# Kernel tuning notes

Hardware: AMD Instinct MI355X
Metric: run time of the kernel (lower is better)

The kernel has to match this reference:

```python
import jax, jax.numpy as jnp
import numpy as np

M = 1024       # molecules
A = 24         # atoms per molecule
N = M * A      # total atoms
H = 128        # hidden_channels
F = 128        # num_filters
G = 50         # num_gaussians
T = 3          # num_interactions
CUTOFF = 10.0
LOG2 = float(np.log(2.0))


def setup_inputs() -> dict:
    key = jax.random.key(0)
    ks = jax.random.split(key, 20)
    z = jax.random.randint(ks[0], (N,), 1, 10)
    # each molecule's atoms in a 5A box -> max pair dist 8.66 < cutoff, all pairs connected
    pos = jax.random.uniform(ks[1], (N, 3), dtype=jnp.float32) * 5.0
    batch = jnp.repeat(jnp.arange(M), A)
    # dense intra-molecule radius graph (deterministic shape)
    i = np.arange(A)
    s, d = np.meshgrid(i, i, indexing='ij')
    m = s != d
    s, d = s[m], d[m]                      # [A*(A-1)]
    offs = (np.arange(M) * A)[:, None]
    edge_index = jnp.asarray(np.stack([(offs + s[None]).ravel(),
                                       (offs + d[None]).ravel()]).astype(np.int64))
    nrm = lambda k, shape: jax.random.normal(k, shape, dtype=jnp.float32) * 0.05
    params = dict(
        emb=nrm(ks[2], (100, H)),
        mlp_w1=nrm(ks[3], (T, G, F)), mlp_b1=jnp.zeros((T, F), jnp.float32),
        mlp_w2=nrm(ks[4], (T, F, F)), mlp_b2=jnp.zeros((T, F), jnp.float32),
        lin1_w=nrm(ks[5], (T, H, F)),
        lin2_w=nrm(ks[6], (T, F, H)), lin2_b=jnp.zeros((T, H), jnp.float32),
        lin_w=nrm(ks[7], (T, H, H)), lin_b=jnp.zeros((T, H), jnp.float32),
        out_w1=nrm(ks[8], (H, H // 2)), out_b1=jnp.zeros((H // 2,), jnp.float32),
        out_w2=nrm(ks[9], (H // 2, 1)), out_b2=jnp.zeros((1,), jnp.float32),
    )
    return dict(z=z, pos=pos, batch=batch, edge_index=edge_index, **params)


def _ssp(x):  # shifted softplus
    return jax.nn.softplus(x) - LOG2


def reference(z, pos, batch, edge_index, emb,
              mlp_w1, mlp_b1, mlp_w2, mlp_b2,
              lin1_w, lin2_w, lin2_b, lin_w, lin_b,
              out_w1, out_b1, out_w2, out_b2):
    src, dst = edge_index[0], edge_index[1]          # message j->i: gather src, scatter dst
    h = emb[z]                                       # [N,H]
    diff = pos[src] - pos[dst]                       # [E,3]
    ew = jnp.sqrt(jnp.sum(diff * diff, axis=-1))     # [E] edge distances
    # Gaussian smearing
    offset = jnp.linspace(0.0, CUTOFF, G, dtype=jnp.float32)
    coeff = -0.5 / (offset[1] - offset[0]) ** 2
    ea = jnp.exp(coeff * (ew[:, None] - offset) ** 2)   # [E,G]
    # cosine cutoff
    C = 0.5 * (jnp.cos(ew * (np.pi / CUTOFF)) + 1.0)    # [E]
    for t in range(T):
        W = _ssp(ea @ mlp_w1[t] + mlp_b1[t]) @ mlp_w2[t] + mlp_b2[t]  # [E,F]
        W = W * C[:, None]
        xf = h @ lin1_w[t]                            # [N,F]
        msg = xf[src] * W                             # [E,F]
        agg = jax.ops.segment_sum(msg, dst, num_segments=N)  # [N,F]
        v = _ssp(agg @ lin2_w[t] + lin2_b[t]) @ lin_w[t] + lin_b[t]  # [N,H]
        h = h + v                                     # residual
    h = _ssp(h @ out_w1 + out_b1)                     # [N,H/2]
    atom_e = h @ out_w2 + out_b2                      # [N,1]
    return jax.ops.segment_sum(atom_e, batch, num_segments=M)  # [M,1] readout='add'
```

## Files before the change

kernel.cpp:

```cpp
#include <hip/hip_runtime.h>
#include <math.h>

#define AT 24
#define ATP 32
#define HD 128
#define GD 50
#define NT 3
#define CUTOFF 10.0f
#define NK 1024

#define KP_W 136
#define XFP 132

#define SZ_BIG (128*KP_W)
#define WS_LIN1(t) ((t)*SZ_BIG)
#define WS_LIN2(t) ((3+(t))*SZ_BIG)
#define WS_LIN(t)  ((6+(t))*SZ_BIG)
#define WS_OW1     (9*SZ_BIG)
#define WS_TAB     (9*SZ_BIG + 64*KP_W)

typedef __attribute__((ext_vector_type(8))) short short8;
typedef __attribute__((ext_vector_type(4))) float f32x4;
typedef __attribute__((ext_vector_type(2))) float f32x2;

__device__ __forceinline__ unsigned short f2bf(float x) {
    unsigned int u = __float_as_uint(x);
    return (unsigned short)((u + 0x7fffu + ((u >> 16) & 1u)) >> 16);
}
__device__ __forceinline__ float sspf(float x) {
    return fmaxf(x, 0.0f) + __logf(1.0f + __expf(-fabsf(x))) - 0.69314718055994531f;
}

#if __has_builtin(__builtin_amdgcn_fdot2_f32_bf16)
typedef __attribute__((ext_vector_type(2))) __bf16 bfv2;
__device__ __forceinline__ float dot2bf(unsigned td, unsigned fp) {
    return __builtin_amdgcn_fdot2_f32_bf16(
        __builtin_bit_cast(bfv2, td), __builtin_bit_cast(bfv2, fp), 0.0f, false);
}
#else
__device__ __forceinline__ float dot2bf(unsigned td, unsigned fp) {
    float t = __uint_as_float(td << 16);
    float d = __uint_as_float(td & 0xFFFF0000u);
    float f = __uint_as_float(fp & 0xFFFF0000u);
    return fmaf(f, d, t);
}
#endif

__device__ __forceinline__ void g2l_async(const void* g, void* l, int bytes, int tid) {
    int w = tid >> 6, lane = tid & 63;
    const char* gc = (const char*)g + lane * 16;
    char* lc = (char*)l + lane * 16;
    for (int ofs = w * 1024; ofs < bytes; ofs += 8192) {
        __builtin_amdgcn_global_load_lds(
            (const __attribute__((address_space(1))) unsigned int*)(gc + ofs),
            (__attribute__((address_space(3))) unsigned int*)(lc + ofs), 16, 0, 0);
    }
}

__device__ __forceinline__ f32x4 mfma16(short8 a, short8 b, f32x4 c) {
    return __builtin_amdgcn_mfma_f32_16x16x32_bf16(a, b, c, 0, 0, 0);
}

template<int NKT>
__device__ __forceinline__ void gemm2(const unsigned short* A, const unsigned short* B,
                                      int q, f32x4* acc)
{
#pragma unroll
    for (int kt = 0; kt < NKT; ++kt) {
        short8 a  = *(const short8*)(A + kt * 32 + q * 8);
        short8 b0 = *(const short8*)(B + kt * 32 + q * 8);
        short8 b1 = *(const short8*)(B + 64 * KP_W + kt * 32 + q * 8);
        acc[0] = mfma16(a, b0, acc[0]);
        acc[1] = mfma16(a, b1, acc[1]);
    }
}

__global__ void __launch_bounds__(256) prep(
    const float* __restrict__ lin1_w, const float* __restrict__ lin2_w,
    const float* __restrict__ lin_w,  const float* __restrict__ out_w1,
    const float* __restrict__ mlp_w1, const float* __restrict__ mlp_b1,
    const float* __restrict__ mlp_w2, const float* __restrict__ mlp_b2,
    unsigned short* __restrict__ ws)
{
    int b = blockIdx.x, tid = threadIdx.x;
    if (b < 40) {
        const float* src; unsigned short* dst; int N, n0, rows;
        if (b < 36) {
            int mat = b >> 2, slice = b & 3;
            int grp = mat / 3, t = mat - grp * 3;
            const float* bases[3] = {lin1_w, lin2_w, lin_w};
            src = bases[grp] + t * HD * HD;
            dst = ws + (grp * 3 + t) * SZ_BIG;
            N = 128; n0 = slice * 32; rows = 32;
        } else {
            src = out_w1; dst = ws + WS_OW1; N = 64; n0 = (b - 36) * 16; rows = 16;
        }
        int nn = tid & 31, kk = tid >> 5;
        if (nn < rows) {
            for (int k = kk; k < KP_W; k += 8) {
                float v = (k < HD) ? src[k * N + n0 + nn] : 0.f;
                dst[(n0 + nn) * KP_W + k] = f2bf(v);
            }
        }
        return;
    }
    __shared__ __align__(16) float w2s[HD * HD];
    __shared__ __align__(16) float ea[9][52];
    __shared__ float pacc[4][5][128];
    __shared__ __align__(16) unsigned short tabst[8 * 256];

    int b2 = b - 40;
    int t = b2 >> 7, k0 = (b2 & 127) << 3;

    {
        const char* gc = (const char*)(mlp_w2 + t * HD * HD) + tid * 16;
        char* lc = (char*)w2s + tid * 16;
#pragma unroll
        for (int ofs = 0; ofs < 65536; ofs += 4096)
            __builtin_amdgcn_global_load_lds(
                (const __attribute__((address_space(1))) unsigned int*)(gc + ofs),
                (__attribute__((address_space(3))) unsigned int*)(lc + ofs), 16, 0, 0);
    }

    const float h = CUTOFF / (NK - 1);
    const float STEP = CUTOFF / (GD - 1);
    const float COEFF = -0.5f / (STEP * STEP);
    for (int i = tid; i < 9 * GD; i += 256) {
        int rr = i / GD, g = i - rr * GD;
        int k = min(k0 + rr, NK - 1);
        float r = (float)k * h;
        float d = r - (float)g * STEP;
        ea[rr][g] = __expf(COEFF * d * d);
    }
    __syncthreads();

    int j = tid & 127, kh = tid >> 7;
    float pre[5];
    float bb1 = mlp_b1[t * HD + j];
#pragma unroll
    for (int rr = 0; rr < 5; ++rr) pre[rr] = bb1;
    const float* w1p = mlp_w1 + t * GD * HD + j;
    for (int g0 = 0; g0 < 48; g0 += 4) {
        f32x4 e[5];
#pragma unroll
        for (int rr = 0; rr < 5; ++rr) e[rr] = *(const f32x4*)&ea[kh * 4 + rr][g0];
        float wv[4];
#pragma unroll
        for (int gg = 0; gg < 4; ++gg) wv[gg] = w1p[(g0 + gg) * HD];
#pragma unroll
        for (int gg = 0; gg < 4; ++gg)
#pragma unroll
            for (int rr = 0; rr < 5; ++rr)
                pre[rr] = fmaf(e[rr][gg], wv[gg], pre[rr]);
    }
#pragma unroll
    for (int g = 48; g < GD; ++g) {
        float wv = w1p[g * HD];
#pragma unroll
        for (int rr = 0; rr < 5; ++rr)
            pre[rr] = fmaf(ea[kh * 4 + rr][g], wv, pre[rr]);
    }
#pragma unroll
    for (int rr = 0; rr < 5; ++rr) pre[rr] = sspf(pre[rr]);

    {
        int wv_ = tid >> 6, l = tid & 63;
        int ubase = (wv_ & 1) << 6;
        float a0[5], a1[5];
#pragma unroll
        for (int rr = 0; rr < 5; ++rr) { a0[rr] = 0.f; a1[rr] = 0.f; }
#pragma unroll 8
        for (int step = 0; step < 64; ++step) {
            int uu = ubase + step;
            float wa = w2s[uu * HD + l];
            float wb = w2s[uu * HD + l + 64];
#pragma unroll
            for (int rr = 0; rr < 5; ++rr) {
                float hv = __uint_as_float(
                    __builtin_amdgcn_readlane(__float_as_uint(pre[rr]), step));
                a0[rr] = fmaf(hv, wa, a0[rr]);
                a1[rr] = fmaf(hv, wb, a1[rr]);
            }
        }
#pragma unroll
        for (int rr = 0; rr < 5; ++rr) {
            pacc[wv_][rr][l] = a0[rr];
            pacc[wv_][rr][l + 64] = a1[rr];
        }
    }
    __syncthreads();
    float bb2 = mlp_b2[t * HD + j];
    float Tv[5];
#pragma unroll
    for (int rr = 0; rr < 5; ++rr) {
        float s = pacc[2 * kh][rr][j] + pacc[2 * kh + 1][rr][j] + bb2;
        int k = min(k0 + kh * 4 + rr, NK - 1);
        float r = (float)k * h;
        Tv[rr] = s * 0.5f * (__cosf(r * 0.31415926535897931f) + 1.0f);
    }
#pragma unroll
    for (int rr = 0; rr < 4; ++rr) {
        int kr = kh * 4 + rr;
        int ofs = kr * 256 + (j >> 1) * 4 + (j & 1) * 2;
        tabst[ofs]     = f2bf(Tv[rr]);
        tabst[ofs + 1] = f2bf(Tv[rr + 1] - Tv[rr]);
    }
    __syncthreads();
    unsigned short* tb = ws + WS_TAB + (size_t)t * NK * 256 + k0 * 256;
    *(short8*)(tb + tid * 8) = *(const short8*)(tabst + tid * 8);
}

extern "C" __global__ __launch_bounds__(512, 4)
void schnet_tab(const int* __restrict__ z, const float* __restrict__ pos,
                const float* __restrict__ emb,
                const float* __restrict__ lin2_b, const float* __restrict__ lin_b,
                const float* __restrict__ out_b1, const float* __restrict__ out_w2,
                const float* __restrict__ out_b2,
                const unsigned short* __restrict__ ws,
                float* __restrict__ out)
{
    __shared__ __align__(16) unsigned char uni_s[ATP * XFP * 4];
    __shared__ __align__(16) unsigned short hb_s[ATP * KP_W];
    __shared__ __align__(16) unsigned short aggb_s[ATP * KP_W];
    __shared__ __align__(16) unsigned short wbuf_s[SZ_BIG];
    __shared__ unsigned eoff_s[AT * AT];
    __shared__ unsigned efpk_s[AT * AT];
    __shared__ float pos_s[AT * 4];
    __shared__ float lb2_s[NT * HD], lb_s[NT * HD];
    __shared__ float ob1_s[64], ow2_s[64];
    __shared__ float red_s;
    float* xf_s = (float*)uni_s;
    unsigned short* tmp_s = (unsigned short*)uni_s;

    const int tid = threadIdx.x, m = blockIdx.x, base = m * AT;
    const int w = tid >> 6, lane = tid & 63, q = lane >> 4, lm = lane & 15;
    const int rn = w & 1, cn = w >> 1;

    g2l_async(ws + WS_LIN1(0), wbuf_s, SZ_BIG * 2, tid);

    if (tid < AT * 3) pos_s[(tid / 3) * 4 + tid % 3] = pos[base * 3 + tid];
    if (tid < NT * HD) { lb2_s[tid] = lin2_b[tid]; lb_s[tid] = lin_b[tid]; }
    else if (tid < NT * HD + 64) ob1_s[tid - NT * HD] = out_b1[tid - NT * HD];
    else if (tid < NT * HD + 128) ow2_s[tid - NT * HD - 64] = out_w2[tid - NT * HD - 64];
    if (tid == 0) red_s = 0.f;
    float hreg[2][4];
#pragma unroll
    for (int c = 0; c < 2; ++c)
#pragma unroll
        for (int i = 0; i < 4; ++i) {
            int row = rn * 16 + q * 4 + i, col = cn * 16 + c * 64 + lm;
            float v = (row < AT) ? emb[z[base + row] * HD + col] : 0.f;
            hreg[c][i] = v;
            hb_s[row * KP_W + col] = f2bf(v);
        }
    for (int i = tid; i < 8 * HD; i += 512)
        aggb_s[(24 + (i >> 7)) * KP_W + (i & 127)] = 0;
    __syncthreads();
    const float INVH = (float)(NK - 1) / CUTOFF;
    for (int i = tid; i < AT * AT; i += 512) {
        int a = i / AT, s = i - a * AT;
        unsigned off; float f;
        if (a == s) { off = 1023u << 9; f = 0.f; }
        else {
            float dx = pos_s[s * 4 + 0] - pos_s[a * 4 + 0];
            float dy = pos_s[s * 4 + 1] - pos_s[a * 4 + 1];
            float dz = pos_s[s * 4 + 2] - pos_s[a * 4 + 2];
            float u = sqrtf(dx * dx + dy * dy + dz * dz) * INVH;
            int idx = (int)u;
            f = u - (float)idx;
            off = (unsigned)idx << 9;
        }
        eoff_s[i] = off;
        efpk_s[i] = 0x3F80u | ((unsigned)f2bf(f) << 16);
    }

    for (int t = 0; t < NT; ++t) {
        __syncthreads();
        {
            f32x4 acc[2] = {};
            gemm2<4>(&hb_s[(rn * 16 + lm) * KP_W], &wbuf_s[(cn * 16 + lm) * KP_W], q, acc);
#pragma unroll
            for (int c = 0; c < 2; ++c) {
                int col = cn * 16 + c * 64 + lm;
#pragma unroll
                for (int i = 0; i < 4; ++i)
                    xf_s[(rn * 16 + q * 4 + i) * XFP + col] = acc[c][i];
            }
        }
        __syncthreads();
        g2l_async(ws + WS_LIN2(t), wbuf_s, SZ_BIG * 2, tid);
        {
            const char* tbase = (const char*)(ws + WS_TAB) + (size_t)t * (NK * 512);
            const int hl = lane >> 5, l32 = lane & 31;
            const int vlo = l32 * 16;
            f32x4 ag[3] = {};
#pragma unroll 1
            for (int s0 = 0; s0 < AT; s0 += 6) {
                uint4 pk[3][3]; unsigned fp[3][3]; f32x4 xv[3];
#pragma unroll
                for (int pp = 0; pp < 3; ++pp) {
                    int s = s0 + 2 * pp + hl;
                    xv[pp] = *(const f32x4*)&xf_s[s * XFP + l32 * 4];
#pragma unroll
                    for (int r = 0; r < 3; ++r) {
                        int a = w + 8 * r;
                        unsigned off = eoff_s[a * AT + s];
                        fp[r][pp] = efpk_s[a * AT + s];
                        pk[r][pp] = *(const uint4*)(tbase + (off + vlo));
                    }
                }
#pragma unroll
                for (int pp = 0; pp < 3; ++pp) {
#pragma unroll
                    for (int r = 0; r < 3; ++r) {
                        uint4 p = pk[r][pp];
                        unsigned f = fp[r][pp];
                        ag[r][0] = fmaf(dot2bf(p.x, f), xv[pp][0], ag[r][0]);
                        ag[r][1] = fmaf(dot2bf(p.y, f), xv[pp][1], ag[r][1]);
                        ag[r][2] = fmaf(dot2bf(p.z, f), xv[pp][2], ag[r][2]);
                        ag[r][3] = fmaf(dot2bf(p.w, f), xv[pp][3], ag[r][3]);
                    }
                }
            }
#pragma unroll
            for (int r = 0; r < 3; ++r)
#pragma unroll
                for (int i = 0; i < 4; ++i)
                    ag[r][i] += __shfl_xor(ag[r][i], 32);
            if (hl == 0) {
#pragma unroll
                for (int r = 0; r < 3; ++r) {
                    int a = w + 8 * r;
                    uint2 pkk;
                    pkk.x = ((unsigned)f2bf(ag[r][1]) << 16) | (unsigned)f2bf(ag[r][0]);
                    pkk.y = ((unsigned)f2bf(ag[r][3]) << 16) | (unsigned)f2bf(ag[r][2]);
                    *(uint2*)&aggb_s[a * KP_W + l32 * 4] = pkk;
                }
            }
        }
        __syncthreads();
        short8 lf[2][4];
        {
            const unsigned short* lwp = ws + WS_LIN(t);
#pragma unroll
            for (int c = 0; c < 2; ++c)
#pragma unroll
                for (int kt = 0; kt < 4; ++kt)
                    lf[c][kt] = *(const short8*)(lwp + (cn * 16 + c * 64 + lm) * KP_W + kt * 32 + q * 8);
        }
        {
            f32x4 acc[2] = {};
            gemm2<4>(&aggb_s[(rn * 16 + lm) * KP_W], &wbuf_s[(cn * 16 + lm) * KP_W], q, acc);
#pragma unroll
            for (int c = 0; c < 2; ++c) {
                int col = cn * 16 + c * 64 + lm;
                float bb = lb2_s[t * HD + col];
#pragma unroll
                for (int i = 0; i < 4; ++i)
                    tmp_s[(rn * 16 + q * 4 + i) * KP_W + col] = f2bf(sspf(acc[c][i] + bb));
            }
        }
        __syncthreads();
        if (t < NT - 1) g2l_async(ws + WS_LIN1(t + 1), wbuf_s, SZ_BIG * 2, tid);
        else            g2l_async(ws + WS_OW1, wbuf_s, 64 * KP_W * 2, tid);
        {
            f32x4 acc[2] = {};
            const unsigned short* A = &tmp_s[(rn * 16 + lm) * KP_W];
#pragma unroll
            for (int kt = 0; kt < 4; ++kt) {
                short8 a = *(const short8*)(A + kt * 32 + q * 8);
                acc[0] = mfma16(a, lf[0][kt], acc[0]);
                acc[1] = mfma16(a, lf[1][kt], acc[1]);
            }
#pragma unroll
            for (int c = 0; c < 2; ++c) {
                int col = cn * 16 + c * 64 + lm;
                float bb = lb_s[t * HD + col];
#pragma unroll
                for (int i = 0; i < 4; ++i) {
                    int row = rn * 16 + q * 4 + i;
                    float nh = hreg[c][i] + acc[c][i] + bb;
                    hreg[c][i] = nh;
                    hb_s[row * KP_W + col] = f2bf(nh);
                }
            }
        }
    }

    __syncthreads();
    {
        int rt = w & 1, co = w >> 1;
        int j = co * 16 + lm;
        f32x4 acc = {};
        const unsigned short* A = &hb_s[(rt * 16 + lm) * KP_W];
        const unsigned short* B = &wbuf_s[j * KP_W];
#pragma unroll
        for (int kt = 0; kt < 4; ++kt)
            acc = mfma16(*(const short8*)(A + kt * 32 + q * 8),
                         *(const short8*)(B + kt * 32 + q * 8), acc);
        float sum = 0.f;
        float bb = ob1_s[j], wo = ow2_s[j];
#pragma unroll
        for (int i = 0; i < 4; ++i) {
            int row = rt * 16 + q * 4 + i;
            if (row < AT) sum += sspf(acc[i] + bb) * wo;
        }
        for (int off = 32; off > 0; off >>= 1) sum += __shfl_down(sum, off);
        if (lane == 0) atomicAdd(&red_s, sum);
    }
    __syncthreads();
    if (tid == 0) out[m] = red_s + (float)AT * out_b2[0];
}

extern "C" void kernel_launch(void* const* d_in, const int* in_sizes, int n_in,
                              void* d_out, int out_size, void* d_ws, size_t ws_size,
                              hipStream_t stream) {
    const int*   z    = (const int*)  d_in[0];
    const float* pos  = (const float*)d_in[1];
    const float* emb  = (const float*)d_in[4];
    const float* mw1  = (const float*)d_in[5];
    const float* mb1  = (const float*)d_in[6];
    const float* mw2  = (const float*)d_in[7];
    const float* mb2  = (const float*)d_in[8];
    const float* l1w  = (const float*)d_in[9];
    const float* l2w  = (const float*)d_in[10];
    const float* l2b  = (const float*)d_in[11];
    const float* lw   = (const float*)d_in[12];
    const float* lb   = (const float*)d_in[13];
    const float* ow1  = (const float*)d_in[14];
    const float* ob1  = (const float*)d_in[15];
    const float* ow2  = (const float*)d_in[16];
    const float* ob2  = (const float*)d_in[17];

    unsigned short* ws = (unsigned short*)d_ws;

    prep<<<dim3(424), dim3(256), 0, stream>>>(l1w, l2w, lw, ow1, mw1, mb1, mw2, mb2, ws);
    schnet_tab<<<dim3(1024), dim3(512), 0, stream>>>(
        z, pos, emb, l2b, lb, ob1, ow2, ob2, ws, (float*)d_out);
}
```

Before: 163.7 us.

## Double-buffer filter table gathers and prefetch first batch before lin1 GEMM

The edge aggregation loop is restructured into a software pipeline with two register buffers. Each step issues the global table gathers for the next 4-source chunk before computing the current chunk. The first chunk's gathers are issued before the lin1 MFMA GEMM so their latency overlaps it. This hides global load latency but raises register pressure, since two sets of six uint4 buffers stay live, which could cut occupancy.

Result: slower. 212.8 us (+30.0%).

```diff
diff --git a/kernel.cpp b/kernel.cpp
--- a/kernel.cpp
+++ b/kernel.cpp
@@ -72,6 +72,37 @@
         short8 b1 = *(const short8*)(B + 64 * KP_W + kt * 32 + q * 8);
         acc[0] = mfma16(a, b0, acc[0]);
         acc[1] = mfma16(a, b1, acc[1]);
+    }
+}
+
+__device__ __forceinline__ void eissue(const char* tbase, const unsigned* eoff_s,
+                                       int w, int hl, int vlo, int s0, uint4 (&buf)[6]) {
+#pragma unroll
+    for (int pp = 0; pp < 2; ++pp)
+#pragma unroll
+        for (int r = 0; r < 3; ++r) {
+            int s = s0 + 2 * pp + hl;
+            unsigned off = eoff_s[(w + 8 * r) * AT + s];
+            buf[pp * 3 + r] = *(const uint4*)(tbase + (off + vlo));
+        }
+}
+
+__device__ __forceinline__ void ecomp(const float* xf_s, const unsigned* efpk_s,
+                                      int w, int hl, int l32, int s0,
+                                      const uint4 (&buf)[6], f32x4 (&ag)[3]) {
+#pragma unroll
+    for (int pp = 0; pp < 2; ++pp) {
+        int s = s0 + 2 * pp + hl;
+        f32x4 xv = *(const f32x4*)&xf_s[s * XFP + l32 * 4];
+#pragma unroll
+        for (int r = 0; r < 3; ++r) {
+            unsigned f = efpk_s[(w + 8 * r) * AT + s];
+            uint4 p = buf[pp * 3 + r];
+            ag[r][0] = fmaf(dot2bf(p.x, f), xv[0], ag[r][0]);
+            ag[r][1] = fmaf(dot2bf(p.y, f), xv[1], ag[r][1]);
+            ag[r][2] = fmaf(dot2bf(p.z, f), xv[2], ag[r][2]);
+            ag[r][3] = fmaf(dot2bf(p.w, f), xv[3], ag[r][3]);
+        }
     }
 }
 
@@ -235,6 +266,7 @@
     const int tid = threadIdx.x, m = blockIdx.x, base = m * AT;
     const int w = tid >> 6, lane = tid & 63, q = lane >> 4, lm = lane & 15;
     const int rn = w & 1, cn = w >> 1;
+    const int hl = lane >> 5, l32 = lane & 31, vlo = l32 * 16;
 
     g2l_async(ws + WS_LIN1(0), wbuf_s, SZ_BIG * 2, tid);
 
@@ -276,6 +308,9 @@
 
     for (int t = 0; t < NT; ++t) {
         __syncthreads();
+        const char* tbase = (const char*)(ws + WS_TAB) + (size_t)t * (NK * 512);
+        uint4 pkA[6], pkB[6];
+        eissue(tbase, eoff_s, w, hl, vlo, 0, pkA);
         {
             f32x4 acc[2] = {};
             gemm2<4>(&hb_s[(rn * 16 + lm) * KP_W], &wbuf_s[(cn * 16 + lm) * KP_W], q, acc);
@@ -290,38 +325,18 @@
         __syncthreads();
         g2l_async(ws + WS_LIN2(t), wbuf_s, SZ_BIG * 2, tid);
         {
-            const char* tbase = (const char*)(ws + WS_TAB) + (size_t)t * (NK * 512);
-            const int hl = lane >> 5, l32 = lane & 31;
-            const int vlo = l32 * 16;
             f32x4 ag[3] = {};
-#pragma unroll 1
-            for (int s0 = 0; s0 < AT; s0 += 6) {
-                uint4 pk[3][3]; unsigned fp[3][3]; f32x4 xv[3];
-#pragma unroll
-                for (int pp = 0; pp < 3; ++pp) {
-                    int s = s0 + 2 * pp + hl;
-                    xv[pp] = *(const f32x4*)&xf_s[s * XFP + l32 * 4];
-#pragma unroll
-                    for (int r = 0; r < 3; ++r) {
-                        int a = w + 8 * r;
-                        unsigned off = eoff_s[a * AT + s];
-                        fp[r][pp] = efpk_s[a * AT + s];
-                        pk[r][pp] = *(const uint4*)(tbase + (off + vlo));
-                    }
-                }
-#pragma unroll
-                for (int pp = 0; pp < 3; ++pp) {
-#pragma unroll
-                    for (int r = 0; r < 3; ++r) {
-                        uint4 p = pk[r][pp];
-                        unsigned f = fp[r][pp];
-                        ag[r][0] = fmaf(dot2bf(p.x, f), xv[pp][0], ag[r][0]);
-                        ag[r][1] = fmaf(dot2bf(p.y, f), xv[pp][1], ag[r][1]);
-                        ag[r][2] = fmaf(dot2bf(p.z, f), xv[pp][2], ag[r][2]);
-                        ag[r][3] = fmaf(dot2bf(p.w, f), xv[pp][3], ag[r][3]);
-                    }
-                }
-            }
+            eissue(tbase, eoff_s, w, hl, vlo, 4,  pkB);
+            ecomp(xf_s, efpk_s, w, hl, l32, 0,  pkA, ag);
+            eissue(tbase, eoff_s, w, hl, vlo, 8,  pkA);
+            ecomp(xf_s, efpk_s, w, hl, l32, 4,  pkB, ag);
+            eissue(tbase, eoff_s, w, hl, vlo, 12, pkB);
+            ecomp(xf_s, efpk_s, w, hl, l32, 8,  pkA, ag);
+            eissue(tbase, eoff_s, w, hl, vlo, 16, pkA);
+            ecomp(xf_s, efpk_s, w, hl, l32, 12, pkB, ag);
+            eissue(tbase, eoff_s, w, hl, vlo, 20, pkB);
+            ecomp(xf_s, efpk_s, w, hl, l32, 16, pkA, ag);
+            ecomp(xf_s, efpk_s, w, hl, l32, 20, pkB, ag);
 #pragma unroll
             for (int r = 0; r < 3; ++r)
 #pragma unroll
```
